# Kernel tuning notes

Hardware: AMD Instinct MI355X
Metric: run time of the kernel (lower is better)

The kernel has to match this reference:

```python
import jax, jax.numpy as jnp
import numpy as np

N = 50000          # nodes
E = 800000         # edges (before self-loops)
IN_DIM = 128
HID = 64           # hidden_dim (per-head out channels)
HEADS = 2
NL = 3             # num_layers of GATConv
CH = HEADS * HID   # 128, per-layer node feature width
LSTM_H = (2 * CH) // 2  # 128, PyG JumpingKnowledge lstm hidden size (num_layers=2)
NEG_SLOPE = 0.2


def setup_inputs() -> dict:
    key = jax.random.key(0)
    ks = jax.random.split(key, 24)
    r = lambda i, shape, s=0.1: jax.random.normal(ks[i], shape, dtype=jnp.float32) * s
    return {
        "x": jax.random.normal(ks[0], (N, IN_DIM), dtype=jnp.float32),
        "edge_index": jax.random.randint(ks[1], (2, E), 0, N),
        "W1": r(2, (CH, IN_DIM)),
        "att1_src": r(3, (HEADS, HID)),
        "att1_dst": r(4, (HEADS, HID)),
        "b1": r(5, (CH,)),
        "Ws": r(6, (NL - 1, CH, CH)),
        "atts_src": r(7, (NL - 1, HEADS, HID)),
        "atts_dst": r(8, (NL - 1, HEADS, HID)),
        "bs": r(9, (NL - 1, CH)),
        "lstm_Wih": r(10, (2, 4 * LSTM_H, CH)),
        "lstm_Whh": r(11, (2, 4 * LSTM_H, LSTM_H)),
        "lstm_bih": r(12, (2, 4 * LSTM_H)),
        "lstm_bhh": r(13, (2, 4 * LSTM_H)),
        "jk_att_w": r(14, (1, 2 * LSTM_H)),
        "jk_att_b": r(15, (1,)),
        "lin1_w": r(16, (HID, CH)),
        "lin1_b": r(17, (HID,)),
        "lin2_w": r(18, (HID, HID + IN_DIM)),
        "lin2_b": r(19, (HID,)),
        "out_w": r(20, (6, HID)),
        "out_b": r(21, (6,)),
    }


def _gat(x, src, dst, W, a_src, a_dst, b):
    # PyG GATConv: linear -> per-head attention logits -> segment softmax over
    # incoming edges -> weighted scatter-add -> concat heads + bias.
    xp = (x @ W.T).reshape(N, HEADS, HID)          # [N,H,C]
    es = jnp.sum(xp * a_src, -1)                   # [N,H]
    ed = jnp.sum(xp * a_dst, -1)                   # [N,H]
    e = jax.nn.leaky_relu(es[src] + ed[dst], NEG_SLOPE)  # [E,H]
    m = jax.ops.segment_max(e, dst, num_segments=N)
    ex = jnp.exp(e - m[dst])
    s = jax.ops.segment_sum(ex, dst, num_segments=N)
    alpha = ex / s[dst]                            # [E,H]
    out = jax.ops.segment_sum(xp[src] * alpha[..., None], dst, num_segments=N)
    return out.reshape(N, CH) + b


def _lstm_dir(seq, Wih, Whh, bih, bhh, reverse):
    # seq: [L, N, CH]; torch gate order (i, f, g, o)
    def step(carry, xt):
        h, c = carry
        g = xt @ Wih.T + bih + h @ Whh.T + bhh
        i, f, gg, o = jnp.split(g, 4, axis=-1)
        c = jax.nn.sigmoid(f) * c + jax.nn.sigmoid(i) * jnp.tanh(gg)
        h = jax.nn.sigmoid(o) * jnp.tanh(c)
        return (h, c), h
    z = jnp.zeros((seq.shape[1], LSTM_H), seq.dtype)
    _, hs = jax.lax.scan(step, (z, z), seq, reverse=reverse)
    return hs  # [L, N, LSTM_H]


def reference(x, edge_index, W1, att1_src, att1_dst, b1, Ws, atts_src, atts_dst, bs,
              lstm_Wih, lstm_Whh, lstm_bih, lstm_bhh, jk_att_w, jk_att_b,
              lin1_w, lin1_b, lin2_w, lin2_b, out_w, out_b):
    loops = jnp.arange(N)
    src = jnp.concatenate([edge_index[0], loops])  # PyG adds self-loops
    dst = jnp.concatenate([edge_index[1], loops])

    h = _gat(x, src, dst, W1, att1_src, att1_dst, b1)  # conv1: no relu on xs[0]
    xs = [h]
    for l in range(NL - 1):
        h = jax.nn.relu(_gat(h, src, dst, Ws[l], atts_src[l], atts_dst[l], bs[l]))
        xs.append(h)

    # JumpingKnowledge 'lstm': biLSTM over layer axis, attention-weighted sum.
    X = jnp.stack(xs, axis=0)                       # [L, N, CH]
    hf = _lstm_dir(X, lstm_Wih[0], lstm_Whh[0], lstm_bih[0], lstm_bhh[0], False)
    hb = _lstm_dir(X, lstm_Wih[1], lstm_Whh[1], lstm_bih[1], lstm_bhh[1], True)
    hcat = jnp.concatenate([hf, hb], -1)            # [L, N, 2*LSTM_H]
    score = (hcat @ jk_att_w.T + jk_att_b)[..., 0]  # [L, N]
    alpha = jax.nn.softmax(score, axis=0)
    jk = jnp.sum(X * alpha[..., None], axis=0)      # [N, CH]

    h1 = jax.nn.relu(jk @ lin1_w.T + lin1_b)        # dropout is identity (eval)
    h2 = jax.nn.relu(jnp.concatenate([h1, x], axis=1) @ lin2_w.T + lin2_b)
    logits = h2 @ out_w.T + out_b
    return jax.nn.log_softmax(logits, axis=1)
```

## Files before the change

### kernel.cpp

```cpp
#include <hip/hip_runtime.h>
#include <math.h>

#define CDIV(a,b) (((a)+(b)-1)/(b))

typedef __attribute__((ext_vector_type(8))) short bfrag;
typedef __attribute__((ext_vector_type(4))) float ffrag;

__device__ inline unsigned short f2bf(float f) {
    unsigned int u = __float_as_uint(f);
    return (unsigned short)((u + 0x7fffu + ((u >> 16) & 1u)) >> 16);
}
__device__ inline float bf2f(unsigned short u) {
    return __uint_as_float(((unsigned int)u) << 16);
}
__device__ inline float sigf(float x) {
    return __builtin_amdgcn_rcpf(1.f + __expf(-x));
}
__device__ inline float tanhfast(float x) {
    float t = __expf(-2.f * fabsf(x));
    float r = (1.f - t) * __builtin_amdgcn_rcpf(1.f + t);
    return copysignf(r, x);
}
__device__ inline int hoff(int row, int k) {
    int sw = ((k >> 3) ^ row) & 15;
    return row * 128 + sw * 8 + (k & 7);
}

__global__ void zero_i32(int* __restrict__ p, int n) {
    int i = blockIdx.x * 256 + threadIdx.x;
    if (i < n) p[i] = 0;
}

__global__ void prep_k(const float* __restrict__ Wih, const float* __restrict__ Whh,
                       const float* __restrict__ bih, const float* __restrict__ bhh,
                       unsigned short* __restrict__ Wp, float* __restrict__ bsum,
                       const float* __restrict__ W1, const float* __restrict__ Ws,
                       const float* __restrict__ l1w, const float* __restrict__ l2w,
                       unsigned short* __restrict__ wb,
                       const float* __restrict__ x, unsigned short* __restrict__ xb, int nx) {
    int i = blockIdx.x * 256 + threadIdx.x;
    if (i < 1024) bsum[i] = bih[i] + bhh[i];
    if (i < 262144) {
        int k = i & 255, j = (i >> 8) & 511, d = i >> 17;
        float v = (k < 128) ? Wih[((size_t)d * 512 + j) * 128 + k]
                            : Whh[((size_t)d * 512 + j) * 128 + (k - 128)];
        Wp[i] = f2bf(v);
        return;
    }
    int i2 = i - 262144;
    if (i2 < 69632) {
        float v;
        if (i2 < 16384)      v = W1[i2];
        else if (i2 < 49152) v = Ws[i2 - 16384];
        else if (i2 < 57344) v = l1w[i2 - 49152];
        else                 v = l2w[i2 - 57344];
        wb[i2] = f2bf(v);
        return;
    }
    int i3 = i2 - 69632;
    if (i3 < nx) xb[i3] = f2bf(x[i3]);
}

__global__ void hist_k(const int* __restrict__ ei, int E, int ET, int* __restrict__ deg) {
    int e = blockIdx.x * 256 + threadIdx.x;
    if (e >= ET) return;
    int d = (e < E) ? ei[E + e] : e - E;
    atomicAdd(deg + d, 1);
}

__global__ __launch_bounds__(256)
void scan1_k(const int* __restrict__ deg, int* __restrict__ row_ptr,
             int* __restrict__ part, int Nn) {
    __shared__ int ls[256];
    int t = threadIdx.x;
    int base = blockIdx.x * 1024 + t * 4;
    int v[4];
    #pragma unroll
    for (int j = 0; j < 4; ++j) v[j] = (base + j < Nn) ? deg[base + j] : 0;
    int s = v[0] + v[1] + v[2] + v[3];
    ls[t] = s;
    __syncthreads();
    for (int off = 1; off < 256; off <<= 1) {
        int o = (t >= off) ? ls[t - off] : 0;
        __syncthreads();
        ls[t] += o;
        __syncthreads();
    }
    int run = ls[t] - s;
    if (t == 255) part[blockIdx.x] = ls[255];
    #pragma unroll
    for (int j = 0; j < 4; ++j) {
        if (base + j < Nn) row_ptr[base + j] = run;
        run += v[j];
    }
}
__global__ void scan2_k(int* __restrict__ part, int nb) {
    int lane = threadIdx.x;
    int v = (lane < nb) ? part[lane] : 0;
    int orig = v;
    for (int off = 1; off < 64; off <<= 1) {
        int o = __shfl_up(v, off);
        if (lane >= off) v += o;
    }
    if (lane < nb) part[lane] = v - orig;
}
__global__ void scan3_k(const int* __restrict__ part, int* __restrict__ row_ptr,
                        int* __restrict__ cursor, int Nn) {
    int i = blockIdx.x * 256 + threadIdx.x;
    if (i >= Nn) return;
    int v = row_ptr[i] + part[i >> 10];
    row_ptr[i] = v;
    cursor[i] = v;
}

__global__ void fill_k(const int* __restrict__ ei, int E, int ET,
                       int* __restrict__ cursor, int* __restrict__ csr_src) {
    int e = blockIdx.x * 256 + threadIdx.x;
    if (e >= ET) return;
    int s, d;
    if (e < E) { s = ei[e]; d = ei[E + e]; } else { s = e - E; d = s; }
    int pos = atomicAdd(cursor + d, 1);
    csr_src[pos] = s;
}

template<int NT, int K, int K1, bool RELU, bool FUSE, bool BFOUT>
__global__ __launch_bounds__(256)
void gemm_mfma_k(const unsigned short* __restrict__ A1, const unsigned short* __restrict__ A2,
                 int ldA2, const unsigned short* __restrict__ Wb, const float* __restrict__ bias,
                 unsigned short* __restrict__ Cb, float* __restrict__ Cf,
                 const float* __restrict__ asl, const float* __restrict__ adl,
                 float* __restrict__ es, float* __restrict__ ed, int M)
{
    int tid = threadIdx.x;
    int wv = tid >> 6, lane = tid & 63;
    int col = lane & 15, kg = lane >> 4;
    int row0 = blockIdx.x * 64 + wv * 16;
    int mrow = row0 + col;
    bool mok = mrow < M;

    ffrag acc[NT];
    #pragma unroll
    for (int t = 0; t < NT; ++t) acc[t] = (ffrag){0.f, 0.f, 0.f, 0.f};

    #pragma unroll
    for (int ks = 0; ks < K / 32; ++ks) {
        int kk = ks * 32 + kg * 8;
        bfrag a = (bfrag){0,0,0,0,0,0,0,0};
        if (mok) {
            if (kk < K1) a = *(const bfrag*)(A1 + (size_t)mrow * K1 + kk);
            else         a = *(const bfrag*)(A2 + (size_t)mrow * ldA2 + (kk - K1));
        }
        #pragma unroll
        for (int t = 0; t < NT; ++t) {
            bfrag b = *(const bfrag*)(Wb + (size_t)(t * 16 + col) * K + kk);
            acc[t] = __builtin_amdgcn_mfma_f32_16x16x32_bf16(a, b, acc[t], 0, 0, 0);
        }
    }

    #pragma unroll
    for (int r = 0; r < 4; ++r) {
        int n = row0 + kg * 4 + r;
        bool ok = n < M;
        float e0 = 0.f, e1 = 0.f, d0 = 0.f, d1 = 0.f;
        #pragma unroll
        for (int t = 0; t < NT; ++t) {
            float v = acc[t][r];
            if (FUSE) {
                int ch = t * 16 + col;
                if (t < NT / 2) { e0 = fmaf(v, asl[ch], e0); d0 = fmaf(v, adl[ch], d0); }
                else            { e1 = fmaf(v, asl[ch], e1); d1 = fmaf(v, adl[ch], d1); }
            }
            if (bias) v += bias[t * 16 + col];
            if (RELU) v = fmaxf(v, 0.f);
            if (ok) {
                if (BFOUT) Cb[(size_t)n * (NT * 16) + t * 16 + col] = f2bf(v);
                else       Cf[(size_t)n * (NT * 16) + t * 16 + col] = v;
            }
        }
        if (FUSE) {
            #pragma unroll
            for (int mk = 1; mk < 16; mk <<= 1) {
                e0 += __shfl_xor(e0, mk); e1 += __shfl_xor(e1, mk);
                d0 += __shfl_xor(d0, mk); d1 += __shfl_xor(d1, mk);
            }
            if (col == 0 && ok) {
                es[n * 2] = e0; es[n * 2 + 1] = e1;
                ed[n * 2] = d0; ed[n * 2 + 1] = d1;
            }
        }
    }
}

__global__ __launch_bounds__(256)
void gat_agg_k(const int* __restrict__ csr_src, const int* __restrict__ row_ptr,
               const int* __restrict__ deg,
               const unsigned short* __restrict__ xpb, const float* __restrict__ es,
               const float* __restrict__ ed, const float* __restrict__ bias,
               unsigned short* __restrict__ out, int Nn, int relu)
{
    int wid = (blockIdx.x * 256 + threadIdx.x) >> 6;
    int lane = threadIdx.x & 63;
    if (wid >= Nn) return;
    int n = wid;
    int beg = row_ptr[n];
    int dn = deg[n];
    float2 edv = *(const float2*)(ed + n * 2);

    int   src_c = 0;
    float z0_c = 0.f, z1_c = 0.f;
    float m0 = -3e38f, m1 = -3e38f, s0 = 0.f, s1 = 0.f;
    for (int i = lane; i < dn; i += 64) {
        int s = csr_src[beg + i];
        float2 e2 = *(const float2*)(es + s * 2);
        float z0 = e2.x + edv.x; z0 = z0 > 0.f ? z0 : 0.2f * z0;
        float z1 = e2.y + edv.y; z1 = z1 > 0.f ? z1 : 0.2f * z1;
        if (i == lane) { src_c = s; z0_c = z0; z1_c = z1; }
        float nm0 = fmaxf(m0, z0);
        s0 = s0 * __expf(m0 - nm0) + __expf(z0 - nm0); m0 = nm0;
        float nm1 = fmaxf(m1, z1);
        s1 = s1 * __expf(m1 - nm1) + __expf(z1 - nm1); m1 = nm1;
    }
    #pragma unroll
    for (int off = 32; off; off >>= 1) {
        float om0 = __shfl_xor(m0, off), os0 = __shfl_xor(s0, off);
        float nm0 = fmaxf(m0, om0);
        s0 = s0 * __expf(m0 - nm0) + os0 * __expf(om0 - nm0); m0 = nm0;
        float om1 = __shfl_xor(m1, off), os1 = __shfl_xor(s1, off);
        float nm1 = fmaxf(m1, om1);
        s1 = s1 * __expf(m1 - nm1) + os1 * __expf(om1 - nm1); m1 = nm1;
    }
    float inv0 = 1.f / s0, inv1 = 1.f / s1;

    float acc0 = 0.f, acc1 = 0.f;
    if (dn <= 64) {
        float a0_c = __expf(z0_c - m0) * inv0;
        float a1_c = __expf(z1_c - m1) * inv1;
        #pragma unroll 8
        for (int i = 0; i < dn; ++i) {
            int s = __shfl(src_c, i);
            float a0 = __shfl(a0_c, i);
            float a1 = __shfl(a1_c, i);
            float aw = (lane < 32) ? a0 : a1;
            unsigned int u = *(const unsigned int*)(xpb + (size_t)s * 128 + 2 * lane);
            acc0 = fmaf(bf2f((unsigned short)(u & 0xffff)), aw, acc0);
            acc1 = fmaf(bf2f((unsigned short)(u >> 16)), aw, acc1);
        }
    } else {
        for (int i = 0; i < dn; ++i) {
            int s = csr_src[beg + i];
            float2 e2 = *(const float2*)(es + s * 2);
            float z0 = e2.x + edv.x; z0 = z0 > 0.f ? z0 : 0.2f * z0;
            float z1 = e2.y + edv.y; z1 = z1 > 0.f ? z1 : 0.2f * z1;
            float a0 = __expf(z0 - m0) * inv0;
            float a1 = __expf(z1 - m1) * inv1;
            float aw = (lane < 32) ? a0 : a1;
            unsigned int u = *(const unsigned int*)(xpb + (size_t)s * 128 + 2 * lane);
            acc0 = fmaf(bf2f((unsigned short)(u & 0xffff)), aw, acc0);
            acc1 = fmaf(bf2f((unsigned short)(u >> 16)), aw, acc1);
        }
    }
    float2 bb = *(const float2*)(bias + 2 * lane);
    float v0 = acc0 + bb.x;
    float v1 = acc1 + bb.y;
    if (relu) { v0 = fmaxf(v0, 0.f); v1 = fmaxf(v1, 0.f); }
    unsigned int o = (unsigned int)f2bf(v0) | ((unsigned int)f2bf(v1) << 16);
    *(unsigned int*)(out + (size_t)n * 128 + 2 * lane) = o;
}

__global__ __launch_bounds__(512)
void lstm_all_k(const unsigned short* __restrict__ X0, const unsigned short* __restrict__ X1,
                const unsigned short* __restrict__ X2,
                const unsigned short* __restrict__ WpB, const float* __restrict__ bsumB,
                const float* __restrict__ jkw, float* __restrict__ score, int Nn, int ntiles)
{
    __shared__ unsigned short h_lds[2][32 * 128];
    __shared__ float sc_s[96];
    int dir = blockIdx.y;
    const unsigned short* Xs0 = dir ? X2 : X0;
    const unsigned short* Xs2 = dir ? X0 : X2;
    const unsigned short* Wp = WpB + (size_t)dir * 512 * 256;
    const float* bsum = bsumB + dir * 512;
    const float* wsc = jkw + dir * 128;
    float* scD = score + (size_t)dir * 3 * Nn;

    int tid = threadIdx.x;
    int wv = tid >> 6, lane = tid & 63;
    int col = lane & 15, kg = lane >> 4;
    int t0 = dir ? 2 : 0;
    int kch = 16 * wv + col;
    float bi = bsum[kch], bf_ = bsum[128 + kch];
    float bg = bsum[256 + kch], bo = bsum[384 + kch];
    float wk = wsc[kch];

    bfrag wreg[4][8];
    #pragma unroll
    for (int g = 0; g < 4; ++g) {
        const unsigned short* wrow = Wp + (size_t)(16 * (8 * g + wv) + col) * 256;
        #pragma unroll
        for (int ks = 0; ks < 8; ++ks)
            wreg[g][ks] = *(const bfrag*)(wrow + ks * 32 + kg * 8);
    }

    for (int tile = blockIdx.x; tile < ntiles; tile += gridDim.x) {
        int node0 = tile * 32;
        float c[2][4] = {};
        if (tid < 96) sc_s[tid] = 0.f;
        __syncthreads();

        #pragma unroll
        for (int i = 0; i < 3; ++i) {
            const unsigned short* Xt = (i == 0) ? Xs0 : ((i == 1) ? X1 : Xs2);
            const unsigned short* h_rd = h_lds[(i + 1) & 1];
            unsigned short* h_wr = h_lds[i & 1];

            ffrag acc[2][4];
            #pragma unroll
            for (int nt = 0; nt < 2; ++nt)
                #pragma unroll
                for (int g = 0; g < 4; ++g) acc[nt][g] = (ffrag){0.f, 0.f, 0.f, 0.f};

            #pragma unroll
            for (int ks = 0; ks < 4; ++ks) {
                int kk = ks * 32 + kg * 8;
                bfrag a0 = *(const bfrag*)(Xt + (size_t)(node0 + col) * 128 + kk);
                bfrag a1 = *(const bfrag*)(Xt + (size_t)(node0 + 16 + col) * 128 + kk);
                #pragma unroll
                for (int g = 0; g < 4; ++g) {
                    acc[0][g] = __builtin_amdgcn_mfma_f32_16x16x32_bf16(a0, wreg[g][ks], acc[0][g], 0, 0, 0);
                    acc[1][g] = __builtin_amdgcn_mfma_f32_16x16x32_bf16(a1, wreg[g][ks], acc[1][g], 0, 0, 0);
                }
            }

            if (i > 0) {
                #pragma unroll
                for (int ks = 4; ks < 8; ++ks) {
                    int kh = (ks - 4) * 32 + kg * 8;
                    bfrag ah0 = *(const bfrag*)&h_rd[hoff(col, kh)];
                    bfrag ah1 = *(const bfrag*)&h_rd[hoff(16 + col, kh)];
                    #pragma unroll
                    for (int g = 0; g < 4; ++g) {
                        acc[0][g] = __builtin_amdgcn_mfma_f32_16x16x32_bf16(ah0, wreg[g][ks], acc[0][g], 0, 0, 0);
                        acc[1][g] = __builtin_amdgcn_mfma_f32_16x16x32_bf16(ah1, wreg[g][ks], acc[1][g], 0, 0, 0);
                    }
                }
            }

            #pragma unroll
            for (int nt = 0; nt < 2; ++nt) {
                #pragma unroll
                for (int r = 0; r < 4; ++r) {
                    float gi = acc[nt][0][r] + bi;
                    float gf = acc[nt][1][r] + bf_;
                    float gg = acc[nt][2][r] + bg;
                    float go = acc[nt][3][r] + bo;
                    float si = sigf(gi);
                    float sf = sigf(gf);
                    float so = sigf(go);
                    float tg = tanhfast(gg);
                    float cn = sf * c[nt][r] + si * tg;
                    float hn = so * tanhfast(cn);
                    c[nt][r] = cn;
                    int nl = nt * 16 + kg * 4 + r;
                    h_wr[hoff(nl, kch)] = f2bf(hn);
                    float v = hn * wk;
                    #pragma unroll
                    for (int mk = 1; mk < 16; mk <<= 1) v += __shfl_xor(v, mk);
                    if (col == 0) atomicAdd(&sc_s[i * 32 + nl], v);
                }
            }
            __syncthreads();
        }

        if (tid < 96) {
            int ii = tid >> 5, nl = tid & 31;
            int t = (ii == 0) ? t0 : ((ii == 1) ? 1 : (2 - t0));
            int n = node0 + nl;
            if (n < Nn) scD[(size_t)t * Nn + n] = sc_s[tid];
        }
        __syncthreads();
    }
}

__global__ void jk_combine_k(const float* __restrict__ scA, const float* __restrict__ scB,
                             const float* __restrict__ jkbias,
                             const unsigned short* __restrict__ x0,
                             const unsigned short* __restrict__ x1, const unsigned short* __restrict__ x2,
                             unsigned short* __restrict__ jkb, int N_) {
    int gid = blockIdx.x * 256 + threadIdx.x;
    int n = gid >> 5;
    if (n >= N_) return;
    int c = (gid & 31) * 4;
    float b = jkbias[0];
    float s0 = b + scA[n] + scB[n];
    float s1 = b + scA[N_ + n] + scB[N_ + n];
    float s2 = b + scA[2*N_ + n] + scB[2*N_ + n];
    float mx = fmaxf(s0, fmaxf(s1, s2));
    float e0 = __expf(s0 - mx), e1 = __expf(s1 - mx), e2 = __expf(s2 - mx);
    float inv = 1.f / (e0 + e1 + e2);
    float a0 = e0 * inv, a1 = e1 * inv, a2 = e2 * inv;
    size_t off = (size_t)n * 128 + c;
    ushort4 u0 = *(const ushort4*)(x0 + off);
    ushort4 u1 = *(const ushort4*)(x1 + off);
    ushort4 u2 = *(const ushort4*)(x2 + off);
    ushort4 o;
    o.x = f2bf(a0*bf2f(u0.x) + a1*bf2f(u1.x) + a2*bf2f(u2.x));
    o.y = f2bf(a0*bf2f(u0.y) + a1*bf2f(u1.y) + a2*bf2f(u2.y));
    o.z = f2bf(a0*bf2f(u0.z) + a1*bf2f(u1.z) + a2*bf2f(u2.z));
    o.w = f2bf(a0*bf2f(u0.w) + a1*bf2f(u1.w) + a2*bf2f(u2.w));
    *(ushort4*)(jkb + off) = o;
}

__global__ void final_out_k(const float* __restrict__ h2, const float* __restrict__ ow,
                            const float* __restrict__ ob, float* __restrict__ out, int N_) {
    int n = blockIdx.x * 256 + threadIdx.x;
    if (n >= N_) return;
    float l[6];
    #pragma unroll
    for (int j = 0; j < 6; ++j) l[j] = ob[j];
    for (int c = 0; c < 64; c += 4) {
        float4 h4 = *(const float4*)(h2 + (size_t)n * 64 + c);
        #pragma unroll
        for (int j = 0; j < 6; ++j) {
            l[j] += h4.x * ow[j*64 + c + 0] + h4.y * ow[j*64 + c + 1]
                  + h4.z * ow[j*64 + c + 2] + h4.w * ow[j*64 + c + 3];
        }
    }
    float mx = l[0];
    #pragma unroll
    for (int j = 1; j < 6; ++j) mx = fmaxf(mx, l[j]);
    float se = 0.f;
    #pragma unroll
    for (int j = 0; j < 6; ++j) se += __expf(l[j] - mx);
    float ls = logf(se) + mx;
    #pragma unroll
    for (int j = 0; j < 6; ++j) out[(size_t)n * 6 + j] = l[j] - ls;
}

extern "C" void kernel_launch(void* const* d_in, const int* in_sizes, int n_in,
                              void* d_out, int out_size, void* d_ws, size_t ws_size,
                              hipStream_t stream) {
    const float* x   = (const float*)d_in[0];
    const int*   ei  = (const int*)d_in[1];
    const float* W1  = (const float*)d_in[2];
    const float* a1s = (const float*)d_in[3];
    const float* a1d = (const float*)d_in[4];
    const float* b1  = (const float*)d_in[5];
    const float* Ws  = (const float*)d_in[6];
    const float* ass = (const float*)d_in[7];
    const float* asd = (const float*)d_in[8];
    const float* bs  = (const float*)d_in[9];
    const float* Wih = (const float*)d_in[10];
    const float* Whh = (const float*)d_in[11];
    const float* bih = (const float*)d_in[12];
    const float* bhh = (const float*)d_in[13];
    const float* jkw = (const float*)d_in[14];
    const float* jkb_b = (const float*)d_in[15];
    const float* l1w = (const float*)d_in[16];
    const float* l1b = (const float*)d_in[17];
    const float* l2w = (const float*)d_in[18];
    const float* l2b = (const float*)d_in[19];
    const float* ow  = (const float*)d_in[20];
    const float* ob  = (const float*)d_in[21];
    float* out = (float*)d_out;

    int Nn = in_sizes[0] / 128;
    int E  = in_sizes[1] / 2;
    int ET = E + Nn;
    size_t Np = ((size_t)Nn + 63) & ~(size_t)63;
    size_t Fp = Np * 128;

    float* w = (float*)d_ws;
    float* es    = w;
    float* ed    = es + 2*Nn;
    float* score = ed + 2*Nn;
    float* bsum  = score + 6*Nn;
    float* h2    = bsum + 1024;
    unsigned short* xb   = (unsigned short*)(h2 + (size_t)Nn*64);
    unsigned short* xpb  = xb + Fp;
    unsigned short* xsb0 = xpb + Fp;
    unsigned short* xsb1 = xsb0 + Fp;
    unsigned short* xsb2 = xsb1 + Fp;
    unsigned short* h1b  = xsb2 + Fp;
    unsigned short* Wp   = h1b + Fp;
    unsigned short* wb   = Wp + 2*512*256;
    int* deg     = (int*)(wb + 69632);
    int* row_ptr = deg + Nn;
    int* cursor  = row_ptr + Nn;
    int* part    = cursor + Nn;
    int* csr_src = part + 64;
    unsigned short* jkb = xpb;

    int nb1 = CDIV(Nn, 1024);
    zero_i32<<<CDIV(Nn, 256), 256, 0, stream>>>(deg, Nn);
    hist_k<<<CDIV(ET, 256), 256, 0, stream>>>(ei, E, ET, deg);
    scan1_k<<<nb1, 256, 0, stream>>>(deg, row_ptr, part, Nn);
    scan2_k<<<1, 64, 0, stream>>>(part, nb1);
    scan3_k<<<CDIV(Nn, 256), 256, 0, stream>>>(part, row_ptr, cursor, Nn);
    fill_k<<<CDIV(ET, 256), 256, 0, stream>>>(ei, E, ET, cursor, csr_src);

    int nprep = 262144 + 69632 + Nn * 128;
    prep_k<<<CDIV(nprep, 256), 256, 0, stream>>>(Wih, Whh, bih, bhh, Wp, bsum,
                                                 W1, Ws, l1w, l2w, wb, x, xb, Nn * 128);

    unsigned short* xsb_arr[3] = {xsb0, xsb1, xsb2};
    int gblk = CDIV(Nn, 64);

    for (int l = 0; l < 3; ++l) {
        const float* asl = (l == 0) ? a1s : ass + (size_t)(l-1) * 128;
        const float* adl = (l == 0) ? a1d : asd + (size_t)(l-1) * 128;
        const float* bl  = (l == 0) ? b1  : bs  + (size_t)(l-1) * 128;
        const unsigned short* Ain = (l == 0) ? xb : xsb_arr[l-1];
        const unsigned short* Wbl = wb + (size_t)l * 16384;
        gemm_mfma_k<8,128,128,false,true,true><<<gblk, 256, 0, stream>>>(
            Ain, Ain, 128, Wbl, nullptr, xpb, nullptr, asl, adl, es, ed, Nn);
        gat_agg_k<<<CDIV(Nn, 4), 256, 0, stream>>>(csr_src, row_ptr, deg, xpb, es, ed, bl,
                                                   xsb_arr[l], Nn, l > 0);
    }

    int ntiles = CDIV(Nn, 32);
    int gx = ntiles < 128 ? ntiles : 128;
    lstm_all_k<<<dim3(gx, 2), 512, 0, stream>>>(xsb0, xsb1, xsb2, Wp, bsum, jkw, score, Nn, ntiles);

    jk_combine_k<<<CDIV(Nn*32, 256), 256, 0, stream>>>(score, score + (size_t)3*Nn, jkb_b,
                                                       xsb0, xsb1, xsb2, jkb, Nn);
    gemm_mfma_k<4,128,128,true,false,true><<<gblk, 256, 0, stream>>>(
        jkb, jkb, 128, wb + 49152, l1b, h1b, nullptr, nullptr, nullptr, nullptr, nullptr, Nn);
    gemm_mfma_k<4,192,64,true,false,false><<<gblk, 256, 0, stream>>>(
        h1b, xb, 128, wb + 57344, l2b, nullptr, h2, nullptr, nullptr, nullptr, nullptr, Nn);
    final_out_k<<<CDIV(Nn, 256), 256, 0, stream>>>(h2, ow, ob, out, Nn);
}
```

Baseline: 605.1 us.

## Process GAT aggregation with 16 lanes per node and 16-byte gathers

Reworks the GAT aggregation kernel so each node is handled by 16 lanes instead of a full 64-lane wavefront, with each lane loading 8 bf16 features per gather as a 16-byte vector. Average degree is about 17, so most of the 64 lanes used in the softmax pass sat idle. Four nodes now share a wavefront and the grid shrinks accordingly. The softmax reduction uses 16-lane shuffles; edges past the first 16 recompute their attention weight from es/ed inside the loop. The cost is 8 accumulators per lane and divergence when degrees differ within a wavefront.

New measurement: 551.4 us. 8.9% less time.

```diff
diff --git a/kernel.cpp b/kernel.cpp
--- a/kernel.cpp
+++ b/kernel.cpp
@@ -198,10 +198,10 @@
                const float* __restrict__ ed, const float* __restrict__ bias,
                unsigned short* __restrict__ out, int Nn, int relu)
 {
-    int wid = (blockIdx.x * 256 + threadIdx.x) >> 6;
-    int lane = threadIdx.x & 63;
-    if (wid >= Nn) return;
-    int n = wid;
+    int tid = threadIdx.x;
+    int l16 = tid & 15;
+    int n = blockIdx.x * 16 + (tid >> 4);
+    if (n >= Nn) return;
     int beg = row_ptr[n];
     int dn = deg[n];
     float2 edv = *(const float2*)(ed + n * 2);
@@ -209,19 +209,19 @@
     int   src_c = 0;
     float z0_c = 0.f, z1_c = 0.f;
     float m0 = -3e38f, m1 = -3e38f, s0 = 0.f, s1 = 0.f;
-    for (int i = lane; i < dn; i += 64) {
+    for (int i = l16; i < dn; i += 16) {
         int s = csr_src[beg + i];
         float2 e2 = *(const float2*)(es + s * 2);
         float z0 = e2.x + edv.x; z0 = z0 > 0.f ? z0 : 0.2f * z0;
         float z1 = e2.y + edv.y; z1 = z1 > 0.f ? z1 : 0.2f * z1;
-        if (i == lane) { src_c = s; z0_c = z0; z1_c = z1; }
+        if (i == l16) { src_c = s; z0_c = z0; z1_c = z1; }
         float nm0 = fmaxf(m0, z0);
         s0 = s0 * __expf(m0 - nm0) + __expf(z0 - nm0); m0 = nm0;
         float nm1 = fmaxf(m1, z1);
         s1 = s1 * __expf(m1 - nm1) + __expf(z1 - nm1); m1 = nm1;
     }
     #pragma unroll
-    for (int off = 32; off; off >>= 1) {
+    for (int off = 8; off; off >>= 1) {
         float om0 = __shfl_xor(m0, off), os0 = __shfl_xor(s0, off);
         float nm0 = fmaxf(m0, om0);
         s0 = s0 * __expf(m0 - nm0) + os0 * __expf(om0 - nm0); m0 = nm0;
@@ -231,40 +231,47 @@
     }
     float inv0 = 1.f / s0, inv1 = 1.f / s1;
 
-    float acc0 = 0.f, acc1 = 0.f;
-    if (dn <= 64) {
-        float a0_c = __expf(z0_c - m0) * inv0;
-        float a1_c = __expf(z1_c - m1) * inv1;
-        #pragma unroll 8
-        for (int i = 0; i < dn; ++i) {
-            int s = __shfl(src_c, i);
-            float a0 = __shfl(a0_c, i);
-            float a1 = __shfl(a1_c, i);
-            float aw = (lane < 32) ? a0 : a1;
-            unsigned int u = *(const unsigned int*)(xpb + (size_t)s * 128 + 2 * lane);
-            acc0 = fmaf(bf2f((unsigned short)(u & 0xffff)), aw, acc0);
-            acc1 = fmaf(bf2f((unsigned short)(u >> 16)), aw, acc1);
-        }
-    } else {
-        for (int i = 0; i < dn; ++i) {
-            int s = csr_src[beg + i];
+    float a0_c = __expf(z0_c - m0) * inv0;
+    float a1_c = __expf(z1_c - m1) * inv1;
+
+    int gbase = (tid & 63) & ~15;
+    float acc[8] = {};
+    for (int i = 0; i < dn; ++i) {
+        int s; float aw;
+        if (i < 16) {
+            int sl = gbase + i;
+            int   sv = __shfl(src_c, sl);
+            float A0 = __shfl(a0_c, sl);
+            float A1 = __shfl(a1_c, sl);
+            s = sv;
+            aw = (l16 < 8) ? A0 : A1;
+        } else {
+            s = csr_src[beg + i];
             float2 e2 = *(const float2*)(es + s * 2);
             float z0 = e2.x + edv.x; z0 = z0 > 0.f ? z0 : 0.2f * z0;
             float z1 = e2.y + edv.y; z1 = z1 > 0.f ? z1 : 0.2f * z1;
-            float a0 = __expf(z0 - m0) * inv0;
-            float a1 = __expf(z1 - m1) * inv1;
-            float aw = (lane < 32) ? a0 : a1;
-            unsigned int u = *(const unsigned int*)(xpb + (size_t)s * 128 + 2 * lane);
-            acc0 = fmaf(bf2f((unsigned short)(u & 0xffff)), aw, acc0);
-            acc1 = fmaf(bf2f((unsigned short)(u >> 16)), aw, acc1);
-        }
-    }
-    float2 bb = *(const float2*)(bias + 2 * lane);
-    float v0 = acc0 + bb.x;
-    float v1 = acc1 + bb.y;
-    if (relu) { v0 = fmaxf(v0, 0.f); v1 = fmaxf(v1, 0.f); }
-    unsigned int o = (unsigned int)f2bf(v0) | ((unsigned int)f2bf(v1) << 16);
-    *(unsigned int*)(out + (size_t)n * 128 + 2 * lane) = o;
+            float aw0 = __expf(z0 - m0) * inv0;
+            float aw1 = __expf(z1 - m1) * inv1;
+            aw = (l16 < 8) ? aw0 : aw1;
+        }
+        bfrag v = *(const bfrag*)(xpb + (size_t)s * 128 + l16 * 8);
+        #pragma unroll
+        for (int j = 0; j < 8; ++j)
+            acc[j] = fmaf(bf2f((unsigned short)v[j]), aw, acc[j]);
+    }
+
+    float4 b0 = *(const float4*)(bias + l16 * 8);
+    float4 b1 = *(const float4*)(bias + l16 * 8 + 4);
+    float vb[8] = {b0.x, b0.y, b0.z, b0.w, b1.x, b1.y, b1.z, b1.w};
+    unsigned int wds[4];
+    #pragma unroll
+    for (int j = 0; j < 4; ++j) {
+        float v0 = acc[2*j]   + vb[2*j];
+        float v1 = acc[2*j+1] + vb[2*j+1];
+        if (relu) { v0 = fmaxf(v0, 0.f); v1 = fmaxf(v1, 0.f); }
+        wds[j] = (unsigned int)f2bf(v0) | ((unsigned int)f2bf(v1) << 16);
+    }
+    *(uint4*)(out + (size_t)n * 128 + l16 * 8) = make_uint4(wds[0], wds[1], wds[2], wds[3]);
 }
 
 __global__ __launch_bounds__(512)
@@ -513,8 +520,8 @@
         const unsigned short* Wbl = wb + (size_t)l * 16384;
         gemm_mfma_k<8,128,128,false,true,true><<<gblk, 256, 0, stream>>>(
             Ain, Ain, 128, Wbl, nullptr, xpb, nullptr, asl, adl, es, ed, Nn);
-        gat_agg_k<<<CDIV(Nn, 4), 256, 0, stream>>>(csr_src, row_ptr, deg, xpb, es, ed, bl,
-                                                   xsb_arr[l], Nn, l > 0);
+        gat_agg_k<<<CDIV(Nn, 16), 256, 0, stream>>>(csr_src, row_ptr, deg, xpb, es, ed, bl,
+                                                    xsb_arr[l], Nn, l > 0);
     }
 
     int ntiles = CDIV(Nn, 32);
```
